# Kernel tuning notes

Measured on AMD Instinct MI355X. Metric: run time of the kernel, lower is better.

## Reference

```python
import jax, jax.numpy as jnp
import numpy as np

SCALE = 1.0  # module scale
# dropout is treated as identity (eval mode / deterministic reference)

def setup_inputs() -> dict:
    key = jax.random.key(0)
    k_x, k_w, k1, k2, k3 = jax.random.split(key, 5)
    B, S, D = 4, 4096, 1280
    x = jax.random.normal(k_x, (B, S, D), dtype=jnp.float32)
    W = jax.random.normal(k_w, (D, D), dtype=jnp.float32) * 0.02  # linear.weight [out, in]
    # kron factors are initialized to identity in the module; perturb slightly
    # so the rotation is non-trivial for correctness testing.
    kron_1 = jnp.eye(4, dtype=jnp.float32) + 0.01 * jax.random.normal(k1, (4, 4), dtype=jnp.float32)
    kron_2 = jnp.eye(8, dtype=jnp.float32) + 0.01 * jax.random.normal(k2, (8, 8), dtype=jnp.float32)
    kron_3 = jnp.eye(40, dtype=jnp.float32) + 0.01 * jax.random.normal(k3, (40, 40), dtype=jnp.float32)
    return {"x": x, "W": W, "kron_1": kron_1, "kron_2": kron_2, "kron_3": kron_3}

def reference(x, W, kron_1, kron_2, kron_3):
    # rotate_matrix = kron(kron(k1, k2), k3)  -> [in, in] = [1280, 1280]
    R = jnp.kron(jnp.kron(kron_1, kron_2), kron_3)
    # rotated_weight = (R @ W^T)^T ; F.linear(x, rotated_weight) = x @ (R @ W^T)
    rotated_weight = (R @ W.T).T  # [out, in]
    out = jnp.einsum('bsd,od->bso', x, rotated_weight)
    return out * SCALE
```

## Files before the change

kernel.cpp:

```cpp
#include <hip/hip_runtime.h>
#include <hip/hip_bf16.h>
#include <stdint.h>

typedef __bf16 bf16x8 __attribute__((ext_vector_type(8)));
typedef float floatx4 __attribute__((ext_vector_type(4)));

__global__ __launch_bounds__(256)
void convert_x(const float* __restrict__ in, __hip_bfloat16* __restrict__ outb) {
    const size_t i = ((size_t)blockIdx.x * 256 + threadIdx.x) * 8;
    const float4 a = *(const float4*)(in + i);
    const float4 b = *(const float4*)(in + i + 4);
    bf16x8 v;
    v[0] = (__bf16)a.x; v[1] = (__bf16)a.y; v[2] = (__bf16)a.z; v[3] = (__bf16)a.w;
    v[4] = (__bf16)b.x; v[5] = (__bf16)b.y; v[6] = (__bf16)b.z; v[7] = (__bf16)b.w;
    *(bf16x8*)((__bf16*)outb + i) = v;
}

__global__ __launch_bounds__(256)
void kron_rotate_w(const float* __restrict__ W,
                   const float* __restrict__ K1,
                   const float* __restrict__ K2,
                   const float* __restrict__ K3,
                   __hip_bfloat16* __restrict__ Wrot) {
    __shared__ float w0[1280];
    __shared__ float t1[1280];
    __shared__ float k3s[1600];
    __shared__ float k2s[64];
    __shared__ float k1s[16];
    const int o   = blockIdx.x;
    const int tid = threadIdx.x;

    for (int i = tid; i < 1280; i += 256) w0[i] = W[o * 1280 + i];
    for (int i = tid; i < 1600; i += 256) k3s[i] = K3[i];
    if (tid < 64) k2s[tid] = K2[tid];
    if (tid < 16) k1s[tid] = K1[tid];
    __syncthreads();

    for (int i = tid; i < 1280; i += 256) {
        const int p = i / 40, d3 = i % 40;
        float acc = 0.f;
        for (int k3 = 0; k3 < 40; ++k3) acc += w0[p * 40 + k3] * k3s[d3 * 40 + k3];
        t1[i] = acc;
    }
    __syncthreads();

    for (int i = tid; i < 1280; i += 256) {
        const int d3 = i % 40, pd = i / 40;
        const int k1 = pd >> 3, d2 = pd & 7;
        float acc = 0.f;
        for (int k2 = 0; k2 < 8; ++k2) acc += t1[(k1 * 8 + k2) * 40 + d3] * k2s[d2 * 8 + k2];
        w0[i] = acc;
    }
    __syncthreads();

    for (int i = tid; i < 1280; i += 256) {
        const int d3 = i % 40, pd = i / 40;
        const int d1 = pd >> 3, d2 = pd & 7;
        float acc = 0.f;
        for (int k1 = 0; k1 < 4; ++k1) acc += w0[(k1 * 8 + d2) * 40 + d3] * k1s[d1 * 4 + k1];
        Wrot[(size_t)o * 1280 + i] = __float2bfloat16(acc);
    }
}

#define BM 128
#define BN 128
#define BK 64
#define LDK 9

__global__ __launch_bounds__(256)
void gemm_bt(const __hip_bfloat16* __restrict__ A,
             const __hip_bfloat16* __restrict__ B,
             float* __restrict__ C,
             int M, int N, int K) {
    __shared__ bf16x8 As[BM * LDK];
    __shared__ bf16x8 Bs[BN * LDK];

    const int tid  = threadIdx.x;
    const int wave = tid >> 6;
    const int lane = tid & 63;
    const int q    = lane >> 4;
    const int r16  = lane & 15;

    const int nTilesN = N / BN;
    const int bn = blockIdx.x % nTilesN;
    const int bm = blockIdx.x / nTilesN;
    const int tileM = bm * BM, tileN = bn * BN;
    const int wm = wave >> 1, wn = wave & 1;

    floatx4 acc[4][4];
#pragma unroll
    for (int i = 0; i < 4; ++i)
#pragma unroll
        for (int j = 0; j < 4; ++j) acc[i][j] = (floatx4){0.f, 0.f, 0.f, 0.f};

    const int row0 = tid >> 3;
    const int slot = tid & 7;

    for (int kt = 0; kt < K; kt += BK) {
        bf16x8 areg[4], breg[4];
#pragma unroll
        for (int t = 0; t < 4; ++t) {
            const int row = t * 32 + row0;
            areg[t] = *(const bf16x8*)(A + (size_t)(tileM + row) * K + kt + slot * 8);
            breg[t] = *(const bf16x8*)(B + (size_t)(tileN + row) * K + kt + slot * 8);
        }
        __syncthreads();
#pragma unroll
        for (int t = 0; t < 4; ++t) {
            const int row = t * 32 + row0;
            As[row * LDK + slot] = areg[t];
            Bs[row * LDK + slot] = breg[t];
        }
        __syncthreads();

#pragma unroll
        for (int s = 0; s < 2; ++s) {
            bf16x8 af[4], bfr[4];
            const int kv = s * 4 + q;
#pragma unroll
            for (int i = 0; i < 4; ++i) {
                const int m = wm * 64 + i * 16 + r16;
                af[i] = As[m * LDK + kv];
                const int n = wn * 64 + i * 16 + r16;
                bfr[i] = Bs[n * LDK + kv];
            }
#pragma unroll
            for (int i = 0; i < 4; ++i)
#pragma unroll
                for (int j = 0; j < 4; ++j)
                    acc[i][j] = __builtin_amdgcn_mfma_f32_16x16x32_bf16(
                        af[i], bfr[j], acc[i][j], 0, 0, 0);
        }
    }

#pragma unroll
    for (int i = 0; i < 4; ++i) {
#pragma unroll
        for (int j = 0; j < 4; ++j) {
            const int col = tileN + wn * 64 + j * 16 + r16;
#pragma unroll
            for (int r = 0; r < 4; ++r) {
                const int row = tileM + wm * 64 + i * 16 + q * 4 + r;
                C[(size_t)row * N + col] = acc[i][j][r];
            }
        }
    }
}

extern "C" void kernel_launch(void* const* d_in, const int* in_sizes, int n_in,
                              void* d_out, int out_size, void* d_ws, size_t ws_size,
                              hipStream_t stream) {
    const float* x  = (const float*)d_in[0];
    const float* W  = (const float*)d_in[1];
    const float* K1 = (const float*)d_in[2];
    const float* K2 = (const float*)d_in[3];
    const float* K3 = (const float*)d_in[4];
    float* out = (float*)d_out;

    const int D = 1280;
    const int M = in_sizes[0] / D;
    const int N = D, K = D;

    __hip_bfloat16* x_bf   = (__hip_bfloat16*)d_ws;
    __hip_bfloat16* Wrot   = x_bf + (size_t)M * K;

    convert_x<<<(M * K) / (256 * 8), 256, 0, stream>>>(x, x_bf);
    kron_rotate_w<<<D, 256, 0, stream>>>(W, K1, K2, K3, Wrot);
    gemm_bt<<<(M / BM) * (N / BN), 256, 0, stream>>>(x_bf, Wrot, out, M, N, K);
}
```

Baseline: 247.3 us.

## Use direct global-to-LDS loads with XOR swizzle and merge prep kernels

The GEMM now loads A and B tiles with global_load_lds straight into an XOR-swizzled LDS layout, replacing the register-staged copy into padded shared memory. This removes the register round-trip and keeps LDS reads free of bank conflicts. The x conversion and weight rotation kernels are merged into one launch to save a launch, and the kron inner loops are vectorised and unrolled. Loads are still not double-buffered, so global latency sits in front of each MFMA phase, and an extra barrier is added per K step.

```diff
diff --git a/kernel.cpp b/kernel.cpp
--- a/kernel.cpp
+++ b/kernel.cpp
@@ -5,30 +5,41 @@
 typedef __bf16 bf16x8 __attribute__((ext_vector_type(8)));
 typedef float floatx4 __attribute__((ext_vector_type(4)));
 
-__global__ __launch_bounds__(256)
-void convert_x(const float* __restrict__ in, __hip_bfloat16* __restrict__ outb) {
-    const size_t i = ((size_t)blockIdx.x * 256 + threadIdx.x) * 8;
-    const float4 a = *(const float4*)(in + i);
-    const float4 b = *(const float4*)(in + i + 4);
-    bf16x8 v;
-    v[0] = (__bf16)a.x; v[1] = (__bf16)a.y; v[2] = (__bf16)a.z; v[3] = (__bf16)a.w;
-    v[4] = (__bf16)b.x; v[5] = (__bf16)b.y; v[6] = (__bf16)b.z; v[7] = (__bf16)b.w;
-    *(bf16x8*)((__bf16*)outb + i) = v;
+__device__ __forceinline__ void async_copy16(void* lds, const void* g) {
+    __builtin_amdgcn_global_load_lds(
+        (const __attribute__((address_space(1))) unsigned int*)g,
+        (__attribute__((address_space(3))) unsigned int*)lds,
+        16, 0, 0);
 }
 
 __global__ __launch_bounds__(256)
-void kron_rotate_w(const float* __restrict__ W,
-                   const float* __restrict__ K1,
-                   const float* __restrict__ K2,
-                   const float* __restrict__ K3,
-                   __hip_bfloat16* __restrict__ Wrot) {
-    __shared__ float w0[1280];
-    __shared__ float t1[1280];
-    __shared__ float k3s[1600];
+void prep(const float* __restrict__ x,
+          const float* __restrict__ W,
+          const float* __restrict__ K1,
+          const float* __restrict__ K2,
+          const float* __restrict__ K3,
+          __hip_bfloat16* __restrict__ x_bf,
+          __hip_bfloat16* __restrict__ Wrot,
+          int nConv) {
+    const int tid = threadIdx.x;
+
+    if ((int)blockIdx.x < nConv) {
+        const size_t i = ((size_t)blockIdx.x * 256 + tid) * 8;
+        const float4 a = *(const float4*)(x + i);
+        const float4 b = *(const float4*)(x + i + 4);
+        bf16x8 v;
+        v[0] = (__bf16)a.x; v[1] = (__bf16)a.y; v[2] = (__bf16)a.z; v[3] = (__bf16)a.w;
+        v[4] = (__bf16)b.x; v[5] = (__bf16)b.y; v[6] = (__bf16)b.z; v[7] = (__bf16)b.w;
+        *(bf16x8*)((__bf16*)x_bf + i) = v;
+        return;
+    }
+
+    const int o = blockIdx.x - nConv;
+    __shared__ __align__(16) float w0[1280];
+    __shared__ __align__(16) float t1[1280];
+    __shared__ __align__(16) float k3s[1600];
     __shared__ float k2s[64];
     __shared__ float k1s[16];
-    const int o   = blockIdx.x;
-    const int tid = threadIdx.x;
 
     for (int i = tid; i < 1280; i += 256) w0[i] = W[o * 1280 + i];
     for (int i = tid; i < 1600; i += 256) k3s[i] = K3[i];
@@ -38,8 +49,14 @@
 
     for (int i = tid; i < 1280; i += 256) {
         const int p = i / 40, d3 = i % 40;
+        const float4* w4 = (const float4*)(w0 + p * 40);
+        const float4* k4 = (const float4*)(k3s + d3 * 40);
         float acc = 0.f;
-        for (int k3 = 0; k3 < 40; ++k3) acc += w0[p * 40 + k3] * k3s[d3 * 40 + k3];
+#pragma unroll
+        for (int t = 0; t < 10; ++t) {
+            const float4 a = w4[t], b = k4[t];
+            acc += a.x * b.x + a.y * b.y + a.z * b.z + a.w * b.w;
+        }
         t1[i] = acc;
     }
     __syncthreads();
@@ -48,6 +65,7 @@
         const int d3 = i % 40, pd = i / 40;
         const int k1 = pd >> 3, d2 = pd & 7;
         float acc = 0.f;
+#pragma unroll
         for (int k2 = 0; k2 < 8; ++k2) acc += t1[(k1 * 8 + k2) * 40 + d3] * k2s[d2 * 8 + k2];
         w0[i] = acc;
     }
@@ -57,6 +75,7 @@
         const int d3 = i % 40, pd = i / 40;
         const int d1 = pd >> 3, d2 = pd & 7;
         float acc = 0.f;
+#pragma unroll
         for (int k1 = 0; k1 < 4; ++k1) acc += w0[(k1 * 8 + d2) * 40 + d3] * k1s[d1 * 4 + k1];
         Wrot[(size_t)o * 1280 + i] = __float2bfloat16(acc);
     }
@@ -65,15 +84,14 @@
 #define BM 128
 #define BN 128
 #define BK 64
-#define LDK 9
 
 __global__ __launch_bounds__(256)
 void gemm_bt(const __hip_bfloat16* __restrict__ A,
              const __hip_bfloat16* __restrict__ B,
              float* __restrict__ C,
              int M, int N, int K) {
-    __shared__ bf16x8 As[BM * LDK];
-    __shared__ bf16x8 Bs[BN * LDK];
+    __shared__ bf16x8 As[1024];
+    __shared__ bf16x8 Bs[1024];
 
     const int tid  = threadIdx.x;
     const int wave = tid >> 6;
@@ -93,23 +111,17 @@
 #pragma unroll
         for (int j = 0; j < 4; ++j) acc[i][j] = (floatx4){0.f, 0.f, 0.f, 0.f};
 
-    const int row0 = tid >> 3;
-    const int slot = tid & 7;
-
     for (int kt = 0; kt < K; kt += BK) {
-        bf16x8 areg[4], breg[4];
 #pragma unroll
         for (int t = 0; t < 4; ++t) {
-            const int row = t * 32 + row0;
-            areg[t] = *(const bf16x8*)(A + (size_t)(tileM + row) * K + kt + slot * 8);
-            breg[t] = *(const bf16x8*)(B + (size_t)(tileN + row) * K + kt + slot * 8);
-        }
-        __syncthreads();
-#pragma unroll
-        for (int t = 0; t < 4; ++t) {
-            const int row = t * 32 + row0;
-            As[row * LDK + slot] = areg[t];
-            Bs[row * LDK + slot] = breg[t];
+            const int g  = wave * 256 + t * 64 + lane;
+            const int m  = g >> 3;
+            const int sl = g & 7;
+            const int kv = sl ^ (m & 7);
+            async_copy16(&As[wave * 256 + t * 64],
+                         A + (size_t)(tileM + m) * K + kt + kv * 8);
+            async_copy16(&Bs[wave * 256 + t * 64],
+                         B + (size_t)(tileN + m) * K + kt + kv * 8);
         }
         __syncthreads();
 
@@ -120,9 +132,9 @@
 #pragma unroll
             for (int i = 0; i < 4; ++i) {
                 const int m = wm * 64 + i * 16 + r16;
-                af[i] = As[m * LDK + kv];
+                af[i] = As[m * 8 + (kv ^ (m & 7))];
                 const int n = wn * 64 + i * 16 + r16;
-                bfr[i] = Bs[n * LDK + kv];
+                bfr[i] = Bs[n * 8 + (kv ^ (n & 7))];
             }
 #pragma unroll
             for (int i = 0; i < 4; ++i)
@@ -131,6 +143,7 @@
                     acc[i][j] = __builtin_amdgcn_mfma_f32_16x16x32_bf16(
                         af[i], bfr[j], acc[i][j], 0, 0, 0);
         }
+        __syncthreads();
     }
 
 #pragma unroll
@@ -161,10 +174,10 @@
     const int M = in_sizes[0] / D;
     const int N = D, K = D;
 
-    __hip_bfloat16* x_bf   = (__hip_bfloat16*)d_ws;
-    __hip_bfloat16* Wrot   = x_bf + (size_t)M * K;
+    __hip_bfloat16* x_bf = (__hip_bfloat16*)d_ws;
+    __hip_bfloat16* Wrot = x_bf + (size_t)M * K;
 
-    convert_x<<<(M * K) / (256 * 8), 256, 0, stream>>>(x, x_bf);
-    kron_rotate_w<<<D, 256, 0, stream>>>(W, K1, K2, K3, Wrot);
+    const int nConv = (M * K) / (256 * 8);
+    prep<<<nConv + D, 256, 0, stream>>>(x, W, K1, K2, K3, x_bf, Wrot, nConv);
     gemm_bt<<<(M / BM) * (N / BN), 256, 0, stream>>>(x_bf, Wrot, out, M, N, K);
 }
```

New measurement: 251.4 us. Within noise of the previous version (+1.6%).
